# Optimization experiments

Hardware: AMD Instinct MI355X
Metric: run time of the kernel (lower is better)

## Reference

```python
import jax, jax.numpy as jnp
import numpy as np

K = 16  # number of neighbors (self excluded), matches init k
NUM_CLASSES = 100


def setup_inputs() -> dict:
    key = jax.random.key(0)
    kx, ky = jax.random.split(key)
    N, D = 8192, 256
    x = jax.random.normal(kx, (N, D), dtype=jnp.float32)
    y = jax.random.randint(ky, (N,), 0, NUM_CLASSES, dtype=jnp.int64)
    return {"x": x, "y": y}


def _knn_loss(x, y):
    N = x.shape[0]
    k = min(K, N - 1)
    # Pairwise squared Euclidean distances via Gram trick: [N, N]
    sq_norms = jnp.sum(x * x, axis=1)
    sq = sq_norms[:, None] + sq_norms[None, :] - 2.0 * (x @ x.T)
    sq = jnp.maximum(sq, 0.0)
    eye = jnp.eye(N, dtype=bool)
    # Keep sqrt grad-safe on the (excluded) diagonal by placing a dummy 1.0 there.
    d = jnp.sqrt(jnp.where(eye, 1.0, sq))  # [N, N] Euclidean distances

    # k nearest neighbors excluding self (BallTree query k+1 then drop col 0).
    d_for_knn = jnp.where(eye, jnp.inf, d)
    _, nn_idx = jax.lax.top_k(-d_for_knn, k)  # [N, k] indices of smallest distances

    # distances = exp(-d); denominator sums over all j != i.
    exp_d = jnp.where(eye, 0.0, jnp.exp(-d))
    denom = jnp.sum(exp_d, axis=1)  # [N]

    # log(exp(-d_in) / denom_i) = -d_in - log(denom_i)
    nn_d = jnp.take_along_axis(d, nn_idx, axis=1)          # [N, k]
    log_p = -nn_d - jnp.log(denom)[:, None]                 # [N, k]

    # Only neighbors with matching label contribute; rows with none are skipped.
    match = (y[nn_idx] == y[:, None]).astype(x.dtype)       # [N, k]
    cnt = jnp.sum(match, axis=1)                            # [N]
    row_mean = jnp.where(cnt > 0, jnp.sum(log_p * match, axis=1) / jnp.maximum(cnt, 1.0), 0.0)
    return -jnp.sum(row_mean) / N


def reference(x, y):
    return _knn_loss(x, y)
```

## Files before the change

kernel.cpp:

```cpp
#include <hip/hip_runtime.h>
#include <hip/hip_fp16.h>


typedef __attribute__((ext_vector_type(8))) short s8v;
typedef __attribute__((ext_vector_type(4))) float f32x4;

#define NROW 8192
#define NK   256

template <bool B> struct BoolC { static constexpr bool value = B; };

#define OFF_DNP  0
#define OFF_NRM  262144
#define OFF_XB   294912
#define OFF_CAND (294912 + 4194304)

__device__ __forceinline__ unsigned short f2bf(float f) {
  unsigned u = __float_as_uint(f);
  return (unsigned short)((u + 0x7FFFu + ((u >> 16) & 1u)) >> 16);
}

__device__ __forceinline__ void gld16(const void* g, void* l) {
  __builtin_amdgcn_global_load_lds(
      (const __attribute__((address_space(1))) unsigned int*)g,
      (__attribute__((address_space(3))) unsigned int*)l, 16, 0, 0);
}

__device__ __forceinline__ unsigned umin32(unsigned a, unsigned b) { return a < b ? a : b; }
__device__ __forceinline__ unsigned umax32(unsigned a, unsigned b) { return a > b ? a : b; }

__global__ __launch_bounds__(256) void k_prep(const float* __restrict__ x,
                                              unsigned short* __restrict__ xb,
                                              float* __restrict__ nrm) {
  const int w = threadIdx.x >> 6, l = threadIdx.x & 63;
  const int r = blockIdx.x * 4 + w;
  const float4 xv = *reinterpret_cast<const float4*>(x + r * NK + l * 4);
  float ns = xv.x * xv.x + xv.y * xv.y + xv.z * xv.z + xv.w * xv.w;
  ns += __shfl_xor(ns, 1);  ns += __shfl_xor(ns, 2);  ns += __shfl_xor(ns, 4);
  ns += __shfl_xor(ns, 8);  ns += __shfl_xor(ns, 16); ns += __shfl_xor(ns, 32);
  if (l == 0) nrm[r] = ns;
  ushort4 bv;
  bv.x = f2bf(xv.x); bv.y = f2bf(xv.y); bv.z = f2bf(xv.z); bv.w = f2bf(xv.w);
  const int gs = (l >> 1) ^ (r & 7);
  *reinterpret_cast<ushort4*>(xb + r * NK + gs * 8 + (l & 1) * 4) = bv;
}

__global__ __launch_bounds__(512, 4) void k_main(const unsigned short* __restrict__ xb,
                                                 const float* __restrict__ nrm,
                                                 float* __restrict__ dnp,
                                                 unsigned* __restrict__ cand) {
  __shared__ __align__(16) unsigned short Bl[2][64 * NK];
  __shared__ float ncsAll[1024];
  __shared__ float dpart[128];
  const int tid = threadIdx.x;
  const int w = tid >> 6, l = tid & 63, l15 = l & 15, l4 = l >> 4;
  const int rb = blockIdx.x >> 3, cs = blockIdx.x & 7;
  const int rowbase = rb * 128 + (w >> 1) * 32;
  const int wcol = (w & 1) * 32;
  const int colslice = cs * 1024;

  if (tid < 128) dpart[tid] = 0.0f;
  ncsAll[tid]       = nrm[colslice + tid];
  ncsAll[tid + 512] = nrm[colslice + 512 + tid];

  s8v A[2][8];
  #pragma unroll
  for (int rf = 0; rf < 2; ++rf) {
    const int rr = rowbase + rf * 16 + l15;
    #pragma unroll
    for (int kf = 0; kf < 8; ++kf) {
      const int g = ((kf << 2) | l4) ^ (rr & 7);
      A[rf][kf] = *reinterpret_cast<const s8v*>(xb + rr * NK + g * 8);
    }
  }
  float nr[2][4], dn[2][4];
  unsigned s0[2][4], s1[2][4];
  #pragma unroll
  for (int rf = 0; rf < 2; ++rf)
    #pragma unroll
    for (int q = 0; q < 4; ++q) {
      nr[rf][q] = nrm[rowbase + rf * 16 + l4 * 4 + q];
      dn[rf][q] = 0.0f;
      s0[rf][q] = 0xFFFFFFFFu;
      s1[rf][q] = 0xFFFFFFFFu;
    }

  auto stage = [&](int buf, int t) {
    const unsigned short* src = xb + (colslice + t * 64) * NK;
    #pragma unroll
    for (int jj = 0; jj < 4; ++jj)
      gld16(src + (jj * 512 + tid) * 8, &Bl[buf][(jj * 512 + w * 64) * 8]);
  };

  const int dtb = rowbase - colslice;
  const int tdw = (dtb >= 0 && dtb < 1024) ? (dtb >> 6) : -1;

  stage(0, 0);
  for (int t = 0; t < 16; ++t) {
    const int cur = t & 1;
    __syncthreads();
    if (t + 1 < 16) stage(cur ^ 1, t + 1);
    const int cbase = colslice + t * 64;
    f32x4 acc[2][2];
    #pragma unroll
    for (int rf = 0; rf < 2; ++rf) {
      f32x4 z = {0.f, 0.f, 0.f, 0.f};
      acc[rf][0] = z; acc[rf][1] = z;
    }
    #pragma unroll
    for (int kf = 0; kf < 8; ++kf) {
      const int gs = ((kf << 2) | l4) ^ (l15 & 7);
      const s8v b0 = *reinterpret_cast<const s8v*>(&Bl[cur][(wcol + l15) * NK + gs * 8]);
      const s8v b1 = *reinterpret_cast<const s8v*>(&Bl[cur][(wcol + 16 + l15) * NK + gs * 8]);
      #pragma unroll
      for (int rf = 0; rf < 2; ++rf) {
        acc[rf][0] = __builtin_amdgcn_mfma_f32_16x16x32_bf16(A[rf][kf], b0, acc[rf][0], 0, 0, 0);
        acc[rf][1] = __builtin_amdgcn_mfma_f32_16x16x32_bf16(A[rf][kf], b1, acc[rf][1], 0, 0, 0);
      }
    }
    const float nc0 = ncsAll[t * 64 + wcol + l15];
    const float nc1 = ncsAll[t * 64 + wcol + 16 + l15];
    const unsigned colg0 = (unsigned)(cbase + wcol + l15);
    const unsigned colg1 = colg0 + 16;
    auto epi = [&](auto dgc) {
      constexpr bool DG = decltype(dgc)::value;
      #pragma unroll
      for (int rf = 0; rf < 2; ++rf)
        #pragma unroll
        for (int q = 0; q < 4; ++q) {
          const unsigned rowg = (unsigned)(rowbase + rf * 16 + l4 * 4 + q);
          float sq0 = fmaf(acc[rf][0][q], -2.0f, nr[rf][q] + nc0);
          float sq1 = fmaf(acc[rf][1][q], -2.0f, nr[rf][q] + nc1);
          if (DG) { sq0 = fmaxf(sq0, 0.0f); sq1 = fmaxf(sq1, 0.0f); }
          const float d0 = __builtin_amdgcn_sqrtf(sq0);
          const float d1 = __builtin_amdgcn_sqrtf(sq1);
          float e0 = __expf(-d0), e1 = __expf(-d1);
          unsigned k0 = ((unsigned)__half_as_ushort(__float2half(d0)) << 16) | colg0;
          unsigned k1 = ((unsigned)__half_as_ushort(__float2half(d1)) << 16) | colg1;
          if (DG) {
            const bool nd0 = (rowg != colg0), nd1 = (rowg != colg1);
            e0 = nd0 ? e0 : 0.0f;          e1 = nd1 ? e1 : 0.0f;
            k0 = nd0 ? k0 : 0xFFFFFFFFu;   k1 = nd1 ? k1 : 0xFFFFFFFFu;
          }
          dn[rf][q] += e0 + e1;
          unsigned ev = umax32(s0[rf][q], k0);
          s0[rf][q] = umin32(s0[rf][q], k0);
          s1[rf][q] = umin32(s1[rf][q], ev);
          ev = umax32(s0[rf][q], k1);
          s0[rf][q] = umin32(s0[rf][q], k1);
          s1[rf][q] = umin32(s1[rf][q], ev);
        }
    };
    if (t == tdw) epi(BoolC<true>{});
    else          epi(BoolC<false>{});
  }
  #pragma unroll
  for (int rf = 0; rf < 2; ++rf)
    #pragma unroll
    for (int q = 0; q < 4; ++q) {
      const int rowg = rowbase + rf * 16 + l4 * 4 + q;
      uint2 pr; pr.x = s0[rf][q]; pr.y = s1[rf][q];
      *reinterpret_cast<uint2*>(&cand[rowg * 512 + cs * 64 + (w & 1) * 32 + l15 * 2]) = pr;
    }
  #pragma unroll
  for (int rf = 0; rf < 2; ++rf)
    #pragma unroll
    for (int q = 0; q < 4; ++q) {
      float vs = dn[rf][q];
      vs += __shfl_xor(vs, 1); vs += __shfl_xor(vs, 2);
      vs += __shfl_xor(vs, 4); vs += __shfl_xor(vs, 8);
      if (l15 == 0) atomicAdd(&dpart[(w >> 1) * 32 + rf * 16 + l4 * 4 + q], vs);
    }
  __syncthreads();
  if (tid < 128) dnp[(rb * 128 + tid) * 8 + cs] = dpart[tid];
}

__global__ __launch_bounds__(256) void k_fin(const unsigned* __restrict__ cand,
                                             const float* __restrict__ dnp,
                                             const int* __restrict__ y,
                                             float* __restrict__ out) {
  const int w = threadIdx.x >> 6, l = threadIdx.x & 63;
  const int r = blockIdx.x * 4 + w;
  unsigned kk[8];
  const uint4 pa = *reinterpret_cast<const uint4*>(cand + r * 512 + l * 8);
  const uint4 pb = *reinterpret_cast<const uint4*>(cand + r * 512 + l * 8 + 4);
  kk[0] = pa.x; kk[1] = pa.y; kk[2] = pa.z; kk[3] = pa.w;
  kk[4] = pb.x; kk[5] = pb.y; kk[6] = pb.z; kk[7] = pb.w;
  unsigned myKey = 0xFFFFFFFFu;
  for (int pp = 0; pp < 16; ++pp) {
    unsigned lm = kk[0];
    #pragma unroll
    for (int j = 1; j < 8; ++j) lm = umin32(lm, kk[j]);
    unsigned m = lm;
    m = umin32(m, __shfl_xor(m, 1));  m = umin32(m, __shfl_xor(m, 2));
    m = umin32(m, __shfl_xor(m, 4));  m = umin32(m, __shfl_xor(m, 8));
    m = umin32(m, __shfl_xor(m, 16)); m = umin32(m, __shfl_xor(m, 32));
    const unsigned long long bal = __ballot(lm == m);
    const int owner = (int)__ffsll(bal) - 1;
    if (l == owner) {
      bool f = false;
      #pragma unroll
      for (int j = 0; j < 8; ++j)
        if (!f && kk[j] == m) { kk[j] = 0xFFFFFFFFu; f = true; }
    }
    if (l == pp) myKey = m;
  }
  float den = 0.0f;
  #pragma unroll
  for (int cs = 0; cs < 8; ++cs) den += dnp[r * 8 + cs];
  const float logden = __logf(den);
  float contrib = 0.0f, cmf = 0.0f;
  if (l < 16 && myKey != 0xFFFFFFFFu) {
    const int col = (int)(myKey & 0x1FFFu);
    const float dd = __half2float(__ushort_as_half((unsigned short)(myKey >> 16)));
    if (y[col] == y[r]) { contrib = -dd - logden; cmf = 1.0f; }
  }
  contrib += __shfl_xor(contrib, 1);  contrib += __shfl_xor(contrib, 2);
  contrib += __shfl_xor(contrib, 4);  contrib += __shfl_xor(contrib, 8);
  contrib += __shfl_xor(contrib, 16); contrib += __shfl_xor(contrib, 32);
  cmf += __shfl_xor(cmf, 1);  cmf += __shfl_xor(cmf, 2);
  cmf += __shfl_xor(cmf, 4);  cmf += __shfl_xor(cmf, 8);
  cmf += __shfl_xor(cmf, 16); cmf += __shfl_xor(cmf, 32);
  if (l == 0 && cmf > 0.0f)
    atomicAdd(out, (contrib / cmf) * (-1.0f / 8192.0f));
}

extern "C" void kernel_launch(void* const* d_in, const int* in_sizes, int n_in,
                              void* d_out, int out_size, void* d_ws, size_t ws_size,
                              hipStream_t stream) {
  const float* x = (const float*)d_in[0];
  const int* y = (const int*)d_in[1];
  float* out = (float*)d_out;
  char* ws = (char*)d_ws;

  float*          dnp  = (float*)(ws + OFF_DNP);
  float*          nrm  = (float*)(ws + OFF_NRM);
  unsigned short* xb   = (unsigned short*)(ws + OFF_XB);
  unsigned*       cand = (unsigned*)(ws + OFF_CAND);

  hipMemsetAsync(d_out, 0, sizeof(float), stream);
  k_prep<<<2048, 256, 0, stream>>>(x, xb, nrm);
  k_main<<<512,  512, 0, stream>>>(xb, nrm, dnp, cand);
  k_fin <<<2048, 256, 0, stream>>>(cand, dnp, y, out);
}
```

Measured before the change: 118.6 us.

## Shrink main blocks to 256 threads, single-buffer LDS, nontemporal candidate I/O

Halves k_main blocks to 64 rows (4 waves) and doubles the grid. The B tile is now single-buffered, with a load-then-sync per step instead of prefetching the next tile. This cuts shared memory per block so more blocks can be resident on each CU, trading away the overlap of global loads with MFMA work. The candidate array is written and read with nontemporal hints to avoid polluting the cache.

```diff
diff --git a/kernel.cpp b/kernel.cpp
--- a/kernel.cpp
+++ b/kernel.cpp
@@ -4,6 +4,8 @@
 
 typedef __attribute__((ext_vector_type(8))) short s8v;
 typedef __attribute__((ext_vector_type(4))) float f32x4;
+typedef __attribute__((ext_vector_type(2))) unsigned u32x2;
+typedef __attribute__((ext_vector_type(4))) unsigned u32x4;
 
 #define NROW 8192
 #define NK   256
@@ -45,23 +47,24 @@
   *reinterpret_cast<ushort4*>(xb + r * NK + gs * 8 + (l & 1) * 4) = bv;
 }
 
-__global__ __launch_bounds__(512, 4) void k_main(const unsigned short* __restrict__ xb,
+__global__ __launch_bounds__(256, 4) void k_main(const unsigned short* __restrict__ xb,
                                                  const float* __restrict__ nrm,
                                                  float* __restrict__ dnp,
                                                  unsigned* __restrict__ cand) {
-  __shared__ __align__(16) unsigned short Bl[2][64 * NK];
+  __shared__ __align__(16) unsigned short Bl[64 * NK];
   __shared__ float ncsAll[1024];
-  __shared__ float dpart[128];
+  __shared__ float dpart[64];
   const int tid = threadIdx.x;
   const int w = tid >> 6, l = tid & 63, l15 = l & 15, l4 = l >> 4;
   const int rb = blockIdx.x >> 3, cs = blockIdx.x & 7;
-  const int rowbase = rb * 128 + (w >> 1) * 32;
+  const int rowbase = rb * 64 + (w >> 1) * 32;
   const int wcol = (w & 1) * 32;
   const int colslice = cs * 1024;
 
-  if (tid < 128) dpart[tid] = 0.0f;
-  ncsAll[tid]       = nrm[colslice + tid];
-  ncsAll[tid + 512] = nrm[colslice + 512 + tid];
+  if (tid < 64) dpart[tid] = 0.0f;
+  #pragma unroll
+  for (int j = 0; j < 4; ++j)
+    ncsAll[tid + j * 256] = nrm[colslice + tid + j * 256];
 
   s8v A[2][8];
   #pragma unroll
@@ -85,21 +88,19 @@
       s1[rf][q] = 0xFFFFFFFFu;
     }
 
-  auto stage = [&](int buf, int t) {
+  auto stage = [&](int t) {
     const unsigned short* src = xb + (colslice + t * 64) * NK;
     #pragma unroll
-    for (int jj = 0; jj < 4; ++jj)
-      gld16(src + (jj * 512 + tid) * 8, &Bl[buf][(jj * 512 + w * 64) * 8]);
+    for (int jj = 0; jj < 8; ++jj)
+      gld16(src + (jj * 256 + tid) * 8, &Bl[(jj * 256 + w * 64) * 8]);
   };
 
   const int dtb = rowbase - colslice;
   const int tdw = (dtb >= 0 && dtb < 1024) ? (dtb >> 6) : -1;
 
-  stage(0, 0);
   for (int t = 0; t < 16; ++t) {
-    const int cur = t & 1;
+    stage(t);
     __syncthreads();
-    if (t + 1 < 16) stage(cur ^ 1, t + 1);
     const int cbase = colslice + t * 64;
     f32x4 acc[2][2];
     #pragma unroll
@@ -110,8 +111,8 @@
     #pragma unroll
     for (int kf = 0; kf < 8; ++kf) {
       const int gs = ((kf << 2) | l4) ^ (l15 & 7);
-      const s8v b0 = *reinterpret_cast<const s8v*>(&Bl[cur][(wcol + l15) * NK + gs * 8]);
-      const s8v b1 = *reinterpret_cast<const s8v*>(&Bl[cur][(wcol + 16 + l15) * NK + gs * 8]);
+      const s8v b0 = *reinterpret_cast<const s8v*>(&Bl[(wcol + l15) * NK + gs * 8]);
+      const s8v b1 = *reinterpret_cast<const s8v*>(&Bl[(wcol + 16 + l15) * NK + gs * 8]);
       #pragma unroll
       for (int rf = 0; rf < 2; ++rf) {
         acc[rf][0] = __builtin_amdgcn_mfma_f32_16x16x32_bf16(A[rf][kf], b0, acc[rf][0], 0, 0, 0);
@@ -153,14 +154,16 @@
     };
     if (t == tdw) epi(BoolC<true>{});
     else          epi(BoolC<false>{});
+    __syncthreads();
   }
   #pragma unroll
   for (int rf = 0; rf < 2; ++rf)
     #pragma unroll
     for (int q = 0; q < 4; ++q) {
       const int rowg = rowbase + rf * 16 + l4 * 4 + q;
-      uint2 pr; pr.x = s0[rf][q]; pr.y = s1[rf][q];
-      *reinterpret_cast<uint2*>(&cand[rowg * 512 + cs * 64 + (w & 1) * 32 + l15 * 2]) = pr;
+      u32x2 pr; pr.x = s0[rf][q]; pr.y = s1[rf][q];
+      __builtin_nontemporal_store(pr,
+          reinterpret_cast<u32x2*>(&cand[rowg * 512 + cs * 64 + (w & 1) * 32 + l15 * 2]));
     }
   #pragma unroll
   for (int rf = 0; rf < 2; ++rf)
@@ -172,7 +175,7 @@
       if (l15 == 0) atomicAdd(&dpart[(w >> 1) * 32 + rf * 16 + l4 * 4 + q], vs);
     }
   __syncthreads();
-  if (tid < 128) dnp[(rb * 128 + tid) * 8 + cs] = dpart[tid];
+  if (tid < 64) dnp[(rb * 64 + tid) * 8 + cs] = dpart[tid];
 }
 
 __global__ __launch_bounds__(256) void k_fin(const unsigned* __restrict__ cand,
@@ -182,8 +185,10 @@
   const int w = threadIdx.x >> 6, l = threadIdx.x & 63;
   const int r = blockIdx.x * 4 + w;
   unsigned kk[8];
-  const uint4 pa = *reinterpret_cast<const uint4*>(cand + r * 512 + l * 8);
-  const uint4 pb = *reinterpret_cast<const uint4*>(cand + r * 512 + l * 8 + 4);
+  const u32x4 pa = __builtin_nontemporal_load(
+      reinterpret_cast<const u32x4*>(cand + r * 512 + l * 8));
+  const u32x4 pb = __builtin_nontemporal_load(
+      reinterpret_cast<const u32x4*>(cand + r * 512 + l * 8 + 4));
   kk[0] = pa.x; kk[1] = pa.y; kk[2] = pa.z; kk[3] = pa.w;
   kk[4] = pb.x; kk[5] = pb.y; kk[6] = pb.z; kk[7] = pb.w;
   unsigned myKey = 0xFFFFFFFFu;
@@ -240,6 +245,6 @@
 
   hipMemsetAsync(d_out, 0, sizeof(float), stream);
   k_prep<<<2048, 256, 0, stream>>>(x, xb, nrm);
-  k_main<<<512,  512, 0, stream>>>(xb, nrm, dnp, cand);
+  k_main<<<1024, 256, 0, stream>>>(xb, nrm, dnp, cand);
   k_fin <<<2048, 256, 0, stream>>>(cand, dnp, y, out);
 }
```

Measured after the change: 113.8 us. 1.04x faster.
